# Kernel optimization log

Measured on AMD Instinct MI355X. Metric: run time of the kernel, lower is better.

## Reference

```python
import jax, jax.numpy as jnp
import numpy as np

NUM_HEADS = 8
WIN = 4
DIM = 256
EPS = 1e-5


def setup_inputs() -> dict:
    key = jax.random.key(0)
    ks = jax.random.split(key, 5)
    B, C, H, W = 2, DIM, 64, 64
    features = jax.random.normal(ks[0], (B, C, H, W), dtype=jnp.float32)
    # Linear(dim, 3*dim): stored as [C, 3C] so y = x @ qkv_w + qkv_b (matches torch x @ W.T + b)
    qkv_w = jax.random.normal(ks[1], (C, 3 * C), dtype=jnp.float32) * 0.02
    qkv_b = jax.random.normal(ks[2], (3 * C,), dtype=jnp.float32) * 0.02
    out_w = jax.random.normal(ks[3], (C, C), dtype=jnp.float32) * 0.02
    out_b = jax.random.normal(ks[4], (C,), dtype=jnp.float32) * 0.02
    ln_w = jnp.ones((C,), dtype=jnp.float32)
    ln_b = jnp.zeros((C,), dtype=jnp.float32)
    return {"features": features, "qkv_w": qkv_w, "qkv_b": qkv_b,
            "out_w": out_w, "out_b": out_b, "ln_w": ln_w, "ln_b": ln_b}


def reference(features, qkv_w, qkv_b, out_w, out_b, ln_w, ln_b):
    ws = WIN
    B, C, H, W = features.shape
    hc, wc = H // ws, W // ws          # windows per col / row (H,W divisible by ws)
    nW = hc * wc
    Tq = ws * ws
    h, d = NUM_HEADS, C // NUM_HEADS

    # --- query windows: replicate torch unfold(k=ws, s=ws).transpose(1,2).reshape(.., Tq, C)
    # torch unfold layout per window is (c, ki, kj); the reshape reinterprets that flat
    # C*ws*ws vector as [ws*ws, C]. A contiguous reshape reproduces this exactly.
    qwin = features.reshape(B, C, hc, ws, wc, ws).transpose(0, 2, 4, 1, 3, 5)  # [B,hc,wc,C,ws,ws]
    q_tok = qwin.reshape(B, nW, Tq, C)
    # LayerNorm(dim) on query tokens only
    mu = q_tok.mean(-1, keepdims=True)
    var = ((q_tok - mu) ** 2).mean(-1, keepdims=True)
    q_tok = (q_tok - mu) / jnp.sqrt(var + EPS) * ln_w + ln_b

    # --- local KV: unfold(k=2*ws, s=ws) on features padded by ws//2 each side
    lk = 2 * ws
    p = ws // 2
    fp = jnp.pad(features, ((0, 0), (0, 0), (p, p), (p, p)))
    rows = jnp.arange(hc)[:, None] * ws + jnp.arange(lk)[None, :]  # [hc, lk]
    cols = jnp.arange(wc)[:, None] * ws + jnp.arange(lk)[None, :]  # [wc, lk]
    loc = fp[:, :, rows[:, None, :, None], cols[None, :, None, :]]  # [B,C,hc,wc,lk,lk]
    loc = loc.transpose(0, 2, 3, 1, 4, 5).reshape(B, nW, lk * lk, C)  # same layout replica
    Ll = lk * lk

    # --- pooled KV (computed once per batch; the torch expand is a pure broadcast)
    mid = features.reshape(B, C, H // 2, 2, W // 2, 2).mean(axis=(3, 5))
    glb = features.reshape(B, C, H // 4, 4, W // 4, 4).mean(axis=(3, 5))
    mid_tok = mid.reshape(B, C, -1).transpose(0, 2, 1)   # [B, Lm, C]
    glb_tok = glb.reshape(B, C, -1).transpose(0, 2, 1)   # [B, Lg, C]
    Lm = mid_tok.shape[1]

    # --- shared qkv projection; queries use only the Q slice, KV use only K/V slices
    q = (q_tok @ qkv_w + qkv_b)[..., :C]

    def kv(t):
        o = t @ qkv_w + qkv_b
        return o[..., C:2 * C], o[..., 2 * C:]

    kl, vl = kv(loc)
    km, vm = kv(mid_tok)
    kg, vg = kv(glb_tok)

    # heads
    q = q.reshape(B, nW, Tq, h, d).transpose(0, 1, 3, 2, 4)           # [B,nW,h,Tq,d]
    kl = kl.reshape(B, nW, Ll, h, d).transpose(0, 1, 3, 2, 4)
    vl = vl.reshape(B, nW, Ll, h, d).transpose(0, 1, 3, 2, 4)
    km = km.reshape(B, Lm, h, d).transpose(0, 2, 1, 3)                # [B,h,Lm,d]
    vm = vm.reshape(B, Lm, h, d).transpose(0, 2, 1, 3)
    kg = kg.reshape(B, -1, h, d).transpose(0, 2, 1, 3)
    vg = vg.reshape(B, -1, h, d).transpose(0, 2, 1, 3)

    scale = 1.0 / np.sqrt(d).astype(np.float32)
    s_l = jnp.einsum('bwhqd,bwhkd->bwhqk', q, kl)
    s_m = jnp.einsum('bwhqd,bhkd->bwhqk', q, km)
    s_g = jnp.einsum('bwhqd,bhkd->bwhqk', q, kg)
    attn = jax.nn.softmax(jnp.concatenate([s_l, s_m, s_g], axis=-1) * scale, axis=-1)
    a_l = attn[..., :Ll]
    a_m = attn[..., Ll:Ll + Lm]
    a_g = attn[..., Ll + Lm:]
    o = (jnp.einsum('bwhqk,bwhkd->bwhqd', a_l, vl)
         + jnp.einsum('bwhqk,bhkd->bwhqd', a_m, vm)
         + jnp.einsum('bwhqk,bhkd->bwhqd', a_g, vg))

    o = o.transpose(0, 1, 3, 2, 4).reshape(B, nW, Tq, C)
    o = o @ out_w + out_b
    # restore spatial layout: view(B,hc,wc,ws,ws,C).permute(0,5,1,3,2,4).view(B,C,H,W)
    o = o.reshape(B, hc, wc, ws, ws, C).transpose(0, 5, 1, 3, 2, 4).reshape(B, C, H, W)
    return o + features
```

## Files before the change

kernel.cpp:

```cpp
#include <hip/hip_runtime.h>
#include <math.h>

#define HWSZ 4096
#define QSCALE_L2E 0.25501988932587245f

typedef __bf16 bf16x2 __attribute__((ext_vector_type(2)));
typedef __bf16 bf16x4 __attribute__((ext_vector_type(4)));
typedef __bf16 bf16x8 __attribute__((ext_vector_type(8)));
typedef float  f32x4  __attribute__((ext_vector_type(4)));

__global__ __launch_bounds__(256) void fused_pre(
    const float* __restrict__ F, const float* __restrict__ lnw,
    const float* __restrict__ lnb, __bf16* __restrict__ qnb,
    float* __restrict__ mid, float* __restrict__ glb,
    const float* __restrict__ Wqkv, const float* __restrict__ Wout,
    __bf16* __restrict__ WT, __bf16* __restrict__ WoT)
{
  __shared__ float sbuf[64*68];
  int u = blockIdx.x;
  int tid = threadIdx.x;
  if (u < 512) {
    float* sm = sbuf;
    int blk = u;
    int b = blk >> 8, wy = (blk >> 4) & 15, t = blk & 15;
    const float* Fb = F + ((size_t)(b*256 + t*16))*HWSZ + (wy*4)*64;
    int py = tid >> 6, x = tid & 63;
    #pragma unroll
    for (int j = 0; j < 16; ++j)
      sm[j*269 + py*67 + x] = Fb[(size_t)j*HWSZ + py*64 + x];
    __syncthreads();
    int wx = tid >> 4, cl = tid & 15;
    float vals[16], s1 = 0.f, s2 = 0.f;
    #pragma unroll
    for (int p = 0; p < 16; ++p) {
      float v = sm[cl*269 + (p >> 2)*67 + wx*4 + (p & 3)];
      vals[p] = v; s1 += v; s2 += v*v;
    }
    #pragma unroll
    for (int m = 1; m < 16; m <<= 1) { s1 += __shfl_xor(s1, m); s2 += __shfl_xor(s2, m); }
    float mean = s1 * (1.f/256.f);
    float var  = s2 * (1.f/256.f) - mean*mean;
    float rstd = rsqrtf(var + 1e-5f);
    __bf16* outp = qnb + (((size_t)(b*256 + wy*16 + wx))*16 + t)*256 + cl*16;
    bf16x8 o0, o1;
    #pragma unroll
    for (int p = 0; p < 8; ++p) {
      o0[p] = (__bf16)((vals[p]  -mean)*rstd*lnw[cl*16+p]   + lnb[cl*16+p]);
      o1[p] = (__bf16)((vals[p+8]-mean)*rstd*lnw[cl*16+p+8] + lnb[cl*16+p+8]);
    }
    *(bf16x8*)outp = o0;
    *(bf16x8*)(outp+8) = o1;
  } else if (u < 1024) {
    int bc = u - 512;
    int gy = tid >> 4, gx = tid & 15;
    const float* p = F + (size_t)bc*HWSZ + (gy*4)*64 + gx*4;
    float4 r0 = *(const float4*)(p);
    float4 r1 = *(const float4*)(p + 64);
    float4 r2 = *(const float4*)(p + 128);
    float4 r3 = *(const float4*)(p + 192);
    float m00 = 0.25f*(r0.x + r0.y + r1.x + r1.y);
    float m01 = 0.25f*(r0.z + r0.w + r1.z + r1.w);
    float m10 = 0.25f*(r2.x + r2.y + r3.x + r3.y);
    float m11 = 0.25f*(r2.z + r2.w + r3.z + r3.w);
    float* mp = mid + (size_t)bc*1024 + (gy*2)*32 + gx*2;
    *(float2*)mp        = make_float2(m00, m01);
    *(float2*)(mp + 32) = make_float2(m10, m11);
    glb[(size_t)bc*256 + gy*16 + gx] = 0.25f*(m00 + m01 + m10 + m11);
  } else {
    float (*T)[68] = (float(*)[68])sbuf;
    int v = u - 1024;
    int bx = v & 15, k0 = (v >> 4)*64;
    int c4 = (tid & 15)*4, rr = tid >> 4;
    const float* W; __bf16* D; int ncols, n0;
    if (bx < 12) { W = Wqkv; D = WT;  ncols = 768; n0 = bx*64; }
    else         { W = Wout; D = WoT; ncols = 256; n0 = (bx-12)*64; }
    #pragma unroll
    for (int p = 0; p < 4; ++p) {
      int row = p*16 + rr;
      float4 vv = *(const float4*)(W + (size_t)(k0+row)*ncols + n0 + c4);
      T[c4+0][row] = vv.x; T[c4+1][row] = vv.y; T[c4+2][row] = vv.z; T[c4+3][row] = vv.w;
    }
    __syncthreads();
    #pragma unroll
    for (int p = 0; p < 4; ++p) {
      int cc = p*16 + rr;
      bf16x4 o;
      o[0] = (__bf16)T[cc][c4+0]; o[1] = (__bf16)T[cc][c4+1];
      o[2] = (__bf16)T[cc][c4+2]; o[3] = (__bf16)T[cc][c4+3];
      *(bf16x4*)(D + (size_t)(n0+cc)*256 + k0 + c4) = o;
    }
  }
}

__global__ __launch_bounds__(256) void mgt_transpose(
    const float* __restrict__ mid, const float* __restrict__ glb,
    __bf16* __restrict__ mgt)
{
  __shared__ float T[64][68];
  int tt = blockIdx.x;
  int tid = threadIdx.x;
  int c4 = (tid & 15)*4, rr = tid >> 4;
  int b = tt / 20, tq = tt % 20;
  int t0 = tq*64, c0 = blockIdx.y*64;
  const float* src; int stride, toff;
  if (t0 < 1024) { src = mid + ((size_t)(b*256 + c0))*1024; stride = 1024; toff = t0; }
  else           { src = glb + ((size_t)(b*256 + c0))*256;  stride = 256;  toff = t0 - 1024; }
  #pragma unroll
  for (int p = 0; p < 4; ++p) {
    int row = p*16 + rr;
    float4 v = *(const float4*)(src + (size_t)row*stride + toff + c4);
    T[c4+0][row] = v.x; T[c4+1][row] = v.y; T[c4+2][row] = v.z; T[c4+3][row] = v.w;
  }
  __syncthreads();
  #pragma unroll
  for (int p = 0; p < 4; ++p) {
    int t2 = p*16 + rr;
    bf16x4 o;
    o[0] = (__bf16)T[t2][c4+0]; o[1] = (__bf16)T[t2][c4+1];
    o[2] = (__bf16)T[t2][c4+2]; o[3] = (__bf16)T[t2][c4+3];
    *(bf16x4*)(mgt + ((size_t)b*1280 + t0 + t2)*256 + c0 + c4) = o;
  }
}

__global__ __launch_bounds__(256) void fused_gemms(
    const float* __restrict__ F, const __bf16* __restrict__ qnb,
    const __bf16* __restrict__ mgt, const __bf16* __restrict__ WT,
    const float* __restrict__ qkvb,
    __bf16* __restrict__ qbf, __bf16* __restrict__ kloc,
    __bf16* __restrict__ vloct, __bf16* __restrict__ kmg,
    __bf16* __restrict__ vmgt)
{
  __shared__ __bf16 Bs[2][16*264];
  int u = blockIdx.x;
  int tid = threadIdx.x;
  int wv = tid >> 6, lane = tid & 63;
  int col = lane & 15, quad = lane >> 4;
  const f32x4 zero = {0.f,0.f,0.f,0.f};

  if (u < 512) {
    int bw = u;
    int b = bw >> 8, w = bw & 255;
    int wy = w >> 4, wx = w & 15;
    int m0 = wv*16;

    bf16x8 af[8];
    int x0 = wx*4 - 2;
    bool p0ok = (wx > 0), p3ok = (wx < 15);
    const float* Fb = F + ((size_t)(b*256 + 4*(m0+col)))*HWSZ;
    #pragma unroll
    for (int kk = 0; kk < 8; ++kk) {
      int r = kk >> 1;
      int y = wy*4 + (kk & 1)*4 + quad - 2;
      bool yok = ((unsigned)y < 64u);
      const float* row = Fb + (size_t)r*HWSZ + y*64 + x0;
      float2 v0 = make_float2(0.f,0.f), v1 = make_float2(0.f,0.f);
      float2 v2 = make_float2(0.f,0.f), v3 = make_float2(0.f,0.f);
      if (yok) {
        if (p0ok) v0 = *(const float2*)(row);
        v1 = *(const float2*)(row + 2);
        v2 = *(const float2*)(row + 4);
        if (p3ok) v3 = *(const float2*)(row + 6);
      }
      af[kk][0] = (__bf16)v0.x; af[kk][1] = (__bf16)v0.y;
      af[kk][2] = (__bf16)v1.x; af[kk][3] = (__bf16)v1.y;
      af[kk][4] = (__bf16)v2.x; af[kk][5] = (__bf16)v2.y;
      af[kk][6] = (__bf16)v3.x; af[kk][7] = (__bf16)v3.y;
    }

    int brow = tid >> 4, bseg = tid & 15;
    const __bf16* wsrc = WT + ((size_t)(256 + brow))*256 + bseg*16;
    __bf16* bd0 = &Bs[0][0] + brow*264 + bseg*16;
    {
      bf16x8 a0 = *(const bf16x8*)wsrc;
      bf16x8 a1 = *(const bf16x8*)(wsrc + 8);
      *(bf16x8*)bd0 = a0;
      *(bf16x8*)(bd0 + 8) = a1;
    }
    bf16x8 g0 = *(const bf16x8*)(wsrc + (size_t)4096);
    bf16x8 g1 = *(const bf16x8*)(wsrc + (size_t)4096 + 8);
    __syncthreads();

    #pragma unroll 1
    for (int nt = 0; nt < 32; ++nt) {
      if (nt < 31) {
        __bf16* d = &Bs[(nt+1) & 1][0] + brow*264 + bseg*16;
        *(bf16x8*)d = g0;
        *(bf16x8*)(d + 8) = g1;
      }
      if (nt < 30) {
        const __bf16* p = wsrc + (size_t)(nt+2)*4096;
        g0 = *(const bf16x8*)p;
        g1 = *(const bf16x8*)(p + 8);
      }
      int n = nt*16 + col;
      float bias_n = qkvb[256 + n];
      const __bf16* Bb = &Bs[nt & 1][0] + col*264 + quad*8;
      f32x4 acc = zero;
      #pragma unroll
      for (int kk = 0; kk < 8; ++kk) {
        bf16x8 bv = *(const bf16x8*)(Bb + kk*32);
        acc = __builtin_amdgcn_mfma_f32_16x16x32_bf16(af[kk], bv, acc, 0, 0, 0);
      }
      if (nt < 16) {
        #pragma unroll
        for (int r = 0; r < 4; ++r)
          kloc[((size_t)bw*64 + m0 + quad*4 + r)*256 + n] = (__bf16)(acc[r] + bias_n);
      } else {
        bf16x4 o;
        #pragma unroll
        for (int r = 0; r < 4; ++r) o[r] = (__bf16)(acc[r] + bias_n);
        *(bf16x4*)(vloct + ((size_t)bw*256 + (n - 256))*64 + m0 + quad*4) = o;
      }
      __syncthreads();
    }
  } else if (u < 768) {
    int blk = u - 512;
    int tb = blk >> 1, nh = blk & 1;
    int n0 = nh*128;
    int m0 = tb*64 + wv*16;

    bf16x8 bq[8];
    const __bf16* qp = qnb + ((size_t)(m0 + col))*256 + quad*8;
    #pragma unroll
    for (int kk = 0; kk < 8; ++kk) bq[kk] = *(const bf16x8*)(qp + kk*32);

    int brow = tid >> 4, bseg = tid & 15;
    const __bf16* wsrc = WT + ((size_t)(n0 + brow))*256 + bseg*16;
    {
      bf16x8 a0 = *(const bf16x8*)wsrc;
      bf16x8 a1 = *(const bf16x8*)(wsrc + 8);
      __bf16* d = &Bs[0][0] + brow*264 + bseg*16;
      *(bf16x8*)d = a0; *(bf16x8*)(d + 8) = a1;
    }
    bf16x8 g0 = *(const bf16x8*)(wsrc + (size_t)4096);
    bf16x8 g1 = *(const bf16x8*)(wsrc + (size_t)4096 + 8);
    __syncthreads();

    #pragma unroll 1
    for (int s = 0; s < 8; ++s) {
      if (s < 7) {
        __bf16* d = &Bs[(s+1) & 1][0] + brow*264 + bseg*16;
        *(bf16x8*)d = g0; *(bf16x8*)(d + 8) = g1;
      }
      if (s < 6) {
        const __bf16* p = wsrc + (size_t)(s+2)*4096;
        g0 = *(const bf16x8*)p; g1 = *(const bf16x8*)(p + 8);
      }
      const __bf16* Ab = &Bs[s & 1][0] + col*264 + quad*8;
      f32x4 acc = zero;
      #pragma unroll
      for (int kk = 0; kk < 8; ++kk) {
        bf16x8 wf = *(const bf16x8*)(Ab + kk*32);
        acc = __builtin_amdgcn_mfma_f32_16x16x32_bf16(wf, bq[kk], acc, 0, 0, 0);
      }
      int nq4 = n0 + s*16 + quad*4;
      float4 b4 = *(const float4*)(qkvb + nq4);
      float bb[4] = {b4.x, b4.y, b4.z, b4.w};
      bf16x4 o;
      #pragma unroll
      for (int r = 0; r < 4; ++r) o[r] = (__bf16)((acc[r]+bb[r])*QSCALE_L2E);
      *(bf16x4*)(qbf + ((size_t)(m0 + col))*256 + nq4) = o;
      __syncthreads();
    }
  } else {
    int v = u - 768;
    int tb = v % 20, nq = (v / 20) & 3, b = v / 80;
    int m0 = tb*64 + wv*16;
    int n0 = nq*128;

    const __bf16* Ab = mgt + ((size_t)b*1280 + m0 + col)*256 + quad*8;
    bf16x8 af[8];
    #pragma unroll
    for (int kk = 0; kk < 8; ++kk) af[kk] = *(const bf16x8*)(Ab + kk*32);

    int brow = tid >> 4, bseg = tid & 15;
    const __bf16* wsrc = WT + ((size_t)(256 + n0 + brow))*256 + bseg*16;
    {
      bf16x8 a0 = *(const bf16x8*)wsrc;
      bf16x8 a1 = *(const bf16x8*)(wsrc + 8);
      __bf16* d = &Bs[0][0] + brow*264 + bseg*16;
      *(bf16x8*)d = a0; *(bf16x8*)(d + 8) = a1;
    }
    bf16x8 g0 = *(const bf16x8*)(wsrc + (size_t)4096);
    bf16x8 g1 = *(const bf16x8*)(wsrc + (size_t)4096 + 8);
    __syncthreads();

    #pragma unroll 1
    for (int s = 0; s < 8; ++s) {
      if (s < 7) {
        __bf16* d = &Bs[(s+1) & 1][0] + brow*264 + bseg*16;
        *(bf16x8*)d = g0; *(bf16x8*)(d + 8) = g1;
      }
      if (s < 6) {
        const __bf16* p = wsrc + (size_t)(s+2)*4096;
        g0 = *(const bf16x8*)p; g1 = *(const bf16x8*)(p + 8);
      }
      int n = n0 + s*16 + col;
      float bias_n = qkvb[256 + n];
      const __bf16* Bb = &Bs[s & 1][0] + col*264 + quad*8;
      f32x4 acc = zero;
      #pragma unroll
      for (int kk = 0; kk < 8; ++kk) {
        bf16x8 bv = *(const bf16x8*)(Bb + kk*32);
        acc = __builtin_amdgcn_mfma_f32_16x16x32_bf16(af[kk], bv, acc, 0, 0, 0);
      }
      if (n < 256) {
        #pragma unroll
        for (int r = 0; r < 4; ++r)
          kmg[((size_t)b*1280 + m0 + quad*4 + r)*256 + n] = (__bf16)(acc[r] + bias_n);
      } else {
        bf16x4 o;
        #pragma unroll
        for (int r = 0; r < 4; ++r) o[r] = (__bf16)(acc[r] + bias_n);
        *(bf16x4*)(vmgt + ((size_t)b*256 + (n - 256))*1280 + m0 + quad*4) = o;
      }
      __syncthreads();
    }
  }
}

__global__ __launch_bounds__(512) void attn_mfma(
    const __bf16* __restrict__ qbf, const __bf16* __restrict__ kloc,
    const __bf16* __restrict__ vloct, const __bf16* __restrict__ kmg,
    const __bf16* __restrict__ vmgt, __bf16* __restrict__ obf)
{
  __shared__ __bf16 Ks[2][64][40];
  __shared__ __bf16 Vs[2][32][72];
  int blk = blockIdx.x;
  int b = blk >> 8, rr = blk & 255;
  int h = rr >> 5, wg = rr & 31;
  int tid = threadIdx.x, wv = tid >> 6, lane = tid & 63;
  int col = lane & 15, quad = lane >> 4;
  int bw = b*256 + wg*8 + wv;

  bool isK = tid < 256;
  int krow = tid >> 2,        kseg = tid & 3;
  int vrow = (tid - 256) >> 3, vseg = (tid - 256) & 7;
  const __bf16* gbase;
  __bf16 *l0, *l1;
  size_t gslab;
  if (isK) {
    gbase = kmg + ((size_t)(b*1280 + krow))*256 + h*32 + kseg*8;
    gslab = (size_t)64*256;
    l0 = &Ks[0][krow][kseg*8]; l1 = &Ks[1][krow][kseg*8];
  } else {
    gbase = vmgt + ((size_t)(b*256 + h*32 + vrow))*1280 + vseg*8;
    gslab = 64;
    l0 = &Vs[0][vrow][vseg*8]; l1 = &Vs[1][vrow][vseg*8];
  }

  bf16x8 aq = *(const bf16x8*)(qbf + ((size_t)(bw*16 + col))*256 + h*32 + quad*8);
  f32x4 O0 = {0.f,0.f,0.f,0.f}, O1 = {0.f,0.f,0.f,0.f};
  const f32x4 zero = {0.f,0.f,0.f,0.f};
  float ls = 0.f;

  bf16x8 sreg = *(const bf16x8*)gbase;

  const __bf16* klocb = kloc  + (size_t)bw*16384 + h*32 + quad*8;
  const __bf16* vlocb = vloct + (size_t)bw*16384 + (size_t)(h*32)*64;
  #pragma unroll
  for (int ch = 0; ch < 2; ++ch) {
    bf16x8 k0 = *(const bf16x8*)(klocb + (size_t)(ch*32 + col)*256);
    bf16x8 k1 = *(const bf16x8*)(klocb + (size_t)(ch*32 + 16 + col)*256);
    bf16x4 va0 = *(const bf16x4*)(vlocb + (size_t)col*64      + ch*32 + quad*4);
    bf16x4 va1 = *(const bf16x4*)(vlocb + (size_t)col*64      + ch*32 + 16 + quad*4);
    bf16x4 vb0 = *(const bf16x4*)(vlocb + (size_t)(16+col)*64 + ch*32 + quad*4);
    bf16x4 vb1 = *(const bf16x4*)(vlocb + (size_t)(16+col)*64 + ch*32 + 16 + quad*4);
    f32x4 S0 = __builtin_amdgcn_mfma_f32_16x16x32_bf16(k0, aq, zero, 0, 0, 0);
    f32x4 S1 = __builtin_amdgcn_mfma_f32_16x16x32_bf16(k1, aq, zero, 0, 0, 0);
    bf16x8 pf;
    #pragma unroll
    for (int r = 0; r < 4; ++r) {
      float p0 = __builtin_amdgcn_exp2f(S0[r]);
      float p1 = __builtin_amdgcn_exp2f(S1[r]);
      ls += p0 + p1;
      pf[r] = (__bf16)p0; pf[4+r] = (__bf16)p1;
    }
    bf16x8 v0 = __builtin_shufflevector(va0, va1, 0,1,2,3,4,5,6,7);
    bf16x8 v1 = __builtin_shufflevector(vb0, vb1, 0,1,2,3,4,5,6,7);
    O0 = __builtin_amdgcn_mfma_f32_16x16x32_bf16(pf, v0, O0, 0, 0, 0);
    O1 = __builtin_amdgcn_mfma_f32_16x16x32_bf16(pf, v1, O1, 0, 0, 0);
  }

  *(bf16x8*)l0 = sreg;
  sreg = *(const bf16x8*)(gbase + gslab);
  __syncthreads();

  #pragma unroll 1
  for (int s = 0; s < 20; ++s) {
    if (s + 1 < 20) {
      __bf16* ld = (s & 1) ? l0 : l1;
      *(bf16x8*)ld = sreg;
      if (s + 2 < 20) sreg = *(const bf16x8*)(gbase + (size_t)(s+2)*gslab);
    }
    const __bf16* Kb = &Ks[s & 1][0][0];
    const __bf16* Vb = &Vs[s & 1][0][0];
    #pragma unroll
    for (int c = 0; c < 2; ++c) {
      bf16x8 k0 = *(const bf16x8*)(Kb + (c*32 + col)*40 + quad*8);
      bf16x8 k1 = *(const bf16x8*)(Kb + (c*32 + 16 + col)*40 + quad*8);
      bf16x4 va0 = *(const bf16x4*)(Vb + (size_t)col*72      + c*32 + quad*4);
      bf16x4 va1 = *(const bf16x4*)(Vb + (size_t)col*72      + c*32 + 16 + quad*4);
      bf16x4 vb0 = *(const bf16x4*)(Vb + (size_t)(16+col)*72 + c*32 + quad*4);
      bf16x4 vb1 = *(const bf16x4*)(Vb + (size_t)(16+col)*72 + c*32 + 16 + quad*4);
      f32x4 S0 = __builtin_amdgcn_mfma_f32_16x16x32_bf16(k0, aq, zero, 0, 0, 0);
      f32x4 S1 = __builtin_amdgcn_mfma_f32_16x16x32_bf16(k1, aq, zero, 0, 0, 0);
      bf16x8 pf;
      #pragma unroll
      for (int r = 0; r < 4; ++r) {
        float p0 = __builtin_amdgcn_exp2f(S0[r]);
        float p1 = __builtin_amdgcn_exp2f(S1[r]);
        ls += p0 + p1;
        pf[r] = (__bf16)p0; pf[4+r] = (__bf16)p1;
      }
      bf16x8 v0 = __builtin_shufflevector(va0, va1, 0,1,2,3,4,5,6,7);
      bf16x8 v1 = __builtin_shufflevector(vb0, vb1, 0,1,2,3,4,5,6,7);
      O0 = __builtin_amdgcn_mfma_f32_16x16x32_bf16(pf, v0, O0, 0, 0, 0);
      O1 = __builtin_amdgcn_mfma_f32_16x16x32_bf16(pf, v1, O1, 0, 0, 0);
    }
    __syncthreads();
  }

  ls += __shfl_xor(ls, 16);
  ls += __shfl_xor(ls, 32);
  __bf16* op = obf + ((size_t)(bw*16) + quad*4)*256 + h*32 + col;
  #pragma unroll
  for (int r = 0; r < 4; ++r) {
    float inv = 1.f / __shfl(ls, quad*4 + r);
    op[(size_t)r*256]      = (__bf16)(O0[r]*inv);
    op[(size_t)r*256 + 16] = (__bf16)(O1[r]*inv);
  }
}

__global__ __launch_bounds__(256) void gemm_out_strip(
    const __bf16* __restrict__ obf, const __bf16* __restrict__ WoT,
    const float* __restrict__ outb, const float* __restrict__ Fres,
    float* __restrict__ Out)
{
  __shared__ __bf16 Bs4[4*16*264];
  __shared__ __bf16 strip[64*264];
  int blk = blockIdx.x;
  int b = blk >> 7, rest = blk & 127;
  int wy = rest >> 3, cq = (rest >> 1) & 3, xh = rest & 1;
  int c0 = cq*64;
  int tid = threadIdx.x, wv = tid >> 6, lane = tid & 63;
  int col = lane & 15, quad = lane >> 4;
  const f32x4 zero = {0.f,0.f,0.f,0.f};

  {
    int brow = tid >> 4, bseg = tid & 15;
    const __bf16* wsrc = WoT + ((size_t)(c0 + brow))*256 + bseg*16;
    #pragma unroll
    for (int s = 0; s < 4; ++s) {
      bf16x8 a0 = *(const bf16x8*)(wsrc + (size_t)s*4096);
      bf16x8 a1 = *(const bf16x8*)(wsrc + (size_t)s*4096 + 8);
      __bf16* d = Bs4 + s*4224 + brow*264 + bseg*16;
      *(bf16x8*)d = a0; *(bf16x8*)(d + 8) = a1;
    }
  }
  __syncthreads();

  #pragma unroll
  for (int i = 0; i < 2; ++i) {
    int wx = xh*8 + wv*2 + i;
    int win = b*256 + wy*16 + wx;
    bf16x8 ao[8];
    const __bf16* op = obf + ((size_t)win*16 + col)*256 + quad*8;
    #pragma unroll
    for (int kk = 0; kk < 8; ++kk) ao[kk] = *(const bf16x8*)(op + kk*32);
    #pragma unroll
    for (int nt = 0; nt < 4; ++nt) {
      const __bf16* Bb = Bs4 + nt*4224 + col*264 + quad*8;
      f32x4 acc = zero;
      #pragma unroll
      for (int kk = 0; kk < 8; ++kk) {
        bf16x8 wf = *(const bf16x8*)(Bb + kk*32);
        acc = __builtin_amdgcn_mfma_f32_16x16x32_bf16(ao[kk], wf, acc, 0, 0, 0);
      }
      bf16x4 o;
      #pragma unroll
      for (int r = 0; r < 4; ++r) o[r] = (__bf16)acc[r];
      *(bf16x4*)&strip[(nt*16+col)*264 + quad*66 + wx*4] = o;
    }
  }
  __syncthreads();
  #pragma unroll
  for (int j = 0; j < 8; ++j) {
    int f4 = j*256 + tid;
    int xq = (f4 & 7) + xh*8, y = (f4 >> 3) & 3, c = f4 >> 5;
    bf16x4 d = *(const bf16x4*)&strip[c*264 + y*66 + xq*4];
    size_t off = ((size_t)(b*256 + c0 + c))*HWSZ + (wy*4 + y)*64 + xq*4;
    float4 r4 = *(const float4*)(Fres + off);
    float bn = outb[c0 + c];
    float4 o;
    o.x = (float)d[0] + bn + r4.x; o.y = (float)d[1] + bn + r4.y;
    o.z = (float)d[2] + bn + r4.z; o.w = (float)d[3] + bn + r4.w;
    *(float4*)(Out + off) = o;
  }
}

extern "C" void kernel_launch(void* const* d_in, const int* in_sizes, int n_in,
                              void* d_out, int out_size, void* d_ws, size_t ws_size,
                              hipStream_t stream) {
  const float* F     = (const float*)d_in[0];
  const float* qkv_w = (const float*)d_in[1];
  const float* qkv_b = (const float*)d_in[2];
  const float* out_w = (const float*)d_in[3];
  const float* out_b = (const float*)d_in[4];
  const float* ln_w  = (const float*)d_in[5];
  const float* ln_b  = (const float*)d_in[6];
  float* out = (float*)d_out;

  __bf16* qnb   = (__bf16*)d_ws;
  __bf16* qbf   = qnb   + 2097152;
  __bf16* obf   = qbf   + 2097152;
  __bf16* kloc  = obf   + 2097152;
  __bf16* vloct = kloc  + 8388608;
  __bf16* kmg   = vloct + 8388608;
  __bf16* vmgt  = kmg   + 655360;
  __bf16* mgt   = vmgt  + 655360;
  __bf16* WT    = mgt   + 655360;
  __bf16* WoT   = WT    + 196608;
  float*  mid   = (float*)(WoT + 65536);
  float*  glb   = mid   + 524288;

  fused_pre<<<1088, 256, 0, stream>>>(F, ln_w, ln_b, qnb, mid, glb,
                                      qkv_w, out_w, WT, WoT);
  mgt_transpose<<<dim3(40, 4), 256, 0, stream>>>(mid, glb, mgt);
  fused_gemms<<<928, 256, 0, stream>>>(F, qnb, mgt, WT, qkv_b,
                                       qbf, kloc, vloct, kmg, vmgt);
  attn_mfma<<<512, 512, 0, stream>>>(qbf, kloc, vloct, kmg, vmgt, obf);
  gemm_out_strip<<<256, 256, 0, stream>>>(obf, WoT, out_b, F, out);
}
```

Baseline: 147.0 us.

## Fuse mgt transpose into GEMM A-loads and process two windows per block

Removes the separate mgt_transpose kernel. The pooled/global KV GEMM blocks now read fp32 mid/glb directly with strided scalar loads and convert to bf16 in registers. The local KV GEMM blocks each handle two adjacent windows, so every B tile staged in shared memory is reused for twice the MFMA work and the grid shrinks. This saves one launch and an intermediate buffer round trip. In exchange the strided scalar global loads are uncoalesced and the doubled A fragments raise register pressure.

```diff
diff --git a/kernel.cpp b/kernel.cpp
--- a/kernel.cpp
+++ b/kernel.cpp
@@ -92,40 +92,10 @@
   }
 }
 
-__global__ __launch_bounds__(256) void mgt_transpose(
-    const float* __restrict__ mid, const float* __restrict__ glb,
-    __bf16* __restrict__ mgt)
-{
-  __shared__ float T[64][68];
-  int tt = blockIdx.x;
-  int tid = threadIdx.x;
-  int c4 = (tid & 15)*4, rr = tid >> 4;
-  int b = tt / 20, tq = tt % 20;
-  int t0 = tq*64, c0 = blockIdx.y*64;
-  const float* src; int stride, toff;
-  if (t0 < 1024) { src = mid + ((size_t)(b*256 + c0))*1024; stride = 1024; toff = t0; }
-  else           { src = glb + ((size_t)(b*256 + c0))*256;  stride = 256;  toff = t0 - 1024; }
-  #pragma unroll
-  for (int p = 0; p < 4; ++p) {
-    int row = p*16 + rr;
-    float4 v = *(const float4*)(src + (size_t)row*stride + toff + c4);
-    T[c4+0][row] = v.x; T[c4+1][row] = v.y; T[c4+2][row] = v.z; T[c4+3][row] = v.w;
-  }
-  __syncthreads();
-  #pragma unroll
-  for (int p = 0; p < 4; ++p) {
-    int t2 = p*16 + rr;
-    bf16x4 o;
-    o[0] = (__bf16)T[t2][c4+0]; o[1] = (__bf16)T[t2][c4+1];
-    o[2] = (__bf16)T[t2][c4+2]; o[3] = (__bf16)T[t2][c4+3];
-    *(bf16x4*)(mgt + ((size_t)b*1280 + t0 + t2)*256 + c0 + c4) = o;
-  }
-}
-
 __global__ __launch_bounds__(256) void fused_gemms(
     const float* __restrict__ F, const __bf16* __restrict__ qnb,
-    const __bf16* __restrict__ mgt, const __bf16* __restrict__ WT,
-    const float* __restrict__ qkvb,
+    const float* __restrict__ mid, const float* __restrict__ glb,
+    const __bf16* __restrict__ WT, const float* __restrict__ qkvb,
     __bf16* __restrict__ qbf, __bf16* __restrict__ kloc,
     __bf16* __restrict__ vloct, __bf16* __restrict__ kmg,
     __bf16* __restrict__ vmgt)
@@ -137,34 +107,37 @@
   int col = lane & 15, quad = lane >> 4;
   const f32x4 zero = {0.f,0.f,0.f,0.f};
 
-  if (u < 512) {
-    int bw = u;
-    int b = bw >> 8, w = bw & 255;
-    int wy = w >> 4, wx = w & 15;
+  if (u < 256) {
+    int b = u >> 7, wpair = u & 127;
+    int wy = wpair >> 3, wx0 = (wpair & 7)*2;
     int m0 = wv*16;
 
-    bf16x8 af[8];
-    int x0 = wx*4 - 2;
-    bool p0ok = (wx > 0), p3ok = (wx < 15);
+    bf16x8 af[2][8];
     const float* Fb = F + ((size_t)(b*256 + 4*(m0+col)))*HWSZ;
     #pragma unroll
-    for (int kk = 0; kk < 8; ++kk) {
-      int r = kk >> 1;
-      int y = wy*4 + (kk & 1)*4 + quad - 2;
-      bool yok = ((unsigned)y < 64u);
-      const float* row = Fb + (size_t)r*HWSZ + y*64 + x0;
-      float2 v0 = make_float2(0.f,0.f), v1 = make_float2(0.f,0.f);
-      float2 v2 = make_float2(0.f,0.f), v3 = make_float2(0.f,0.f);
-      if (yok) {
-        if (p0ok) v0 = *(const float2*)(row);
-        v1 = *(const float2*)(row + 2);
-        v2 = *(const float2*)(row + 4);
-        if (p3ok) v3 = *(const float2*)(row + 6);
-      }
-      af[kk][0] = (__bf16)v0.x; af[kk][1] = (__bf16)v0.y;
-      af[kk][2] = (__bf16)v1.x; af[kk][3] = (__bf16)v1.y;
-      af[kk][4] = (__bf16)v2.x; af[kk][5] = (__bf16)v2.y;
-      af[kk][6] = (__bf16)v3.x; af[kk][7] = (__bf16)v3.y;
+    for (int wi = 0; wi < 2; ++wi) {
+      int wx = wx0 + wi;
+      int x0 = wx*4 - 2;
+      bool p0ok = (wx > 0), p3ok = (wx < 15);
+      #pragma unroll
+      for (int kk = 0; kk < 8; ++kk) {
+        int r = kk >> 1;
+        int y = wy*4 + (kk & 1)*4 + quad - 2;
+        bool yok = ((unsigned)y < 64u);
+        const float* row = Fb + (size_t)r*HWSZ + y*64 + x0;
+        float2 v0 = make_float2(0.f,0.f), v1 = make_float2(0.f,0.f);
+        float2 v2 = make_float2(0.f,0.f), v3 = make_float2(0.f,0.f);
+        if (yok) {
+          if (p0ok) v0 = *(const float2*)(row);
+          v1 = *(const float2*)(row + 2);
+          v2 = *(const float2*)(row + 4);
+          if (p3ok) v3 = *(const float2*)(row + 6);
+        }
+        af[wi][kk][0] = (__bf16)v0.x; af[wi][kk][1] = (__bf16)v0.y;
+        af[wi][kk][2] = (__bf16)v1.x; af[wi][kk][3] = (__bf16)v1.y;
+        af[wi][kk][4] = (__bf16)v2.x; af[wi][kk][5] = (__bf16)v2.y;
+        af[wi][kk][6] = (__bf16)v3.x; af[wi][kk][7] = (__bf16)v3.y;
+      }
     }
 
     int brow = tid >> 4, bseg = tid & 15;
@@ -195,26 +168,34 @@
       int n = nt*16 + col;
       float bias_n = qkvb[256 + n];
       const __bf16* Bb = &Bs[nt & 1][0] + col*264 + quad*8;
-      f32x4 acc = zero;
+      f32x4 acc0 = zero, acc1 = zero;
       #pragma unroll
       for (int kk = 0; kk < 8; ++kk) {
         bf16x8 bv = *(const bf16x8*)(Bb + kk*32);
-        acc = __builtin_amdgcn_mfma_f32_16x16x32_bf16(af[kk], bv, acc, 0, 0, 0);
-      }
+        acc0 = __builtin_amdgcn_mfma_f32_16x16x32_bf16(af[0][kk], bv, acc0, 0, 0, 0);
+        acc1 = __builtin_amdgcn_mfma_f32_16x16x32_bf16(af[1][kk], bv, acc1, 0, 0, 0);
+      }
+      size_t bw0 = (size_t)(b*256 + wy*16 + wx0);
       if (nt < 16) {
         #pragma unroll
-        for (int r = 0; r < 4; ++r)
-          kloc[((size_t)bw*64 + m0 + quad*4 + r)*256 + n] = (__bf16)(acc[r] + bias_n);
+        for (int r = 0; r < 4; ++r) {
+          kloc[(bw0*64       + m0 + quad*4 + r)*256 + n] = (__bf16)(acc0[r] + bias_n);
+          kloc[((bw0+1)*64   + m0 + quad*4 + r)*256 + n] = (__bf16)(acc1[r] + bias_n);
+        }
       } else {
-        bf16x4 o;
+        bf16x4 o0, o1;
         #pragma unroll
-        for (int r = 0; r < 4; ++r) o[r] = (__bf16)(acc[r] + bias_n);
-        *(bf16x4*)(vloct + ((size_t)bw*256 + (n - 256))*64 + m0 + quad*4) = o;
+        for (int r = 0; r < 4; ++r) {
+          o0[r] = (__bf16)(acc0[r] + bias_n);
+          o1[r] = (__bf16)(acc1[r] + bias_n);
+        }
+        *(bf16x4*)(vloct + (bw0*256     + (n - 256))*64 + m0 + quad*4) = o0;
+        *(bf16x4*)(vloct + ((bw0+1)*256 + (n - 256))*64 + m0 + quad*4) = o1;
       }
       __syncthreads();
     }
-  } else if (u < 768) {
-    int blk = u - 512;
+  } else if (u < 512) {
+    int blk = u - 256;
     int tb = blk >> 1, nh = blk & 1;
     int n0 = nh*128;
     int m0 = tb*64 + wv*16;
@@ -263,15 +244,29 @@
       __syncthreads();
     }
   } else {
-    int v = u - 768;
+    int v = u - 512;
     int tb = v % 20, nq = (v / 20) & 3, b = v / 80;
     int m0 = tb*64 + wv*16;
     int n0 = nq*128;
 
-    const __bf16* Ab = mgt + ((size_t)b*1280 + m0 + col)*256 + quad*8;
     bf16x8 af[8];
-    #pragma unroll
-    for (int kk = 0; kk < 8; ++kk) af[kk] = *(const bf16x8*)(Ab + kk*32);
+    if (tb < 16) {
+      const float* Abase = mid + ((size_t)(b*256))*1024 + (m0 + col);
+      #pragma unroll
+      for (int kk = 0; kk < 8; ++kk) {
+        #pragma unroll
+        for (int j = 0; j < 8; ++j)
+          af[kk][j] = (__bf16)Abase[(size_t)(kk*32 + quad*8 + j)*1024];
+      }
+    } else {
+      const float* Abase = glb + ((size_t)(b*256))*256 + (m0 - 1024 + col);
+      #pragma unroll
+      for (int kk = 0; kk < 8; ++kk) {
+        #pragma unroll
+        for (int j = 0; j < 8; ++j)
+          af[kk][j] = (__bf16)Abase[(size_t)(kk*32 + quad*8 + j)*256];
+      }
+    }
 
     int brow = tid >> 4, bseg = tid & 15;
     const __bf16* wsrc = WT + ((size_t)(256 + n0 + brow))*256 + bseg*16;
@@ -518,16 +513,14 @@
   __bf16* vloct = kloc  + 8388608;
   __bf16* kmg   = vloct + 8388608;
   __bf16* vmgt  = kmg   + 655360;
-  __bf16* mgt   = vmgt  + 655360;
-  __bf16* WT    = mgt   + 655360;
+  __bf16* WT    = vmgt  + 655360;
   __bf16* WoT   = WT    + 196608;
   float*  mid   = (float*)(WoT + 65536);
   float*  glb   = mid   + 524288;
 
   fused_pre<<<1088, 256, 0, stream>>>(F, ln_w, ln_b, qnb, mid, glb,
                                       qkv_w, out_w, WT, WoT);
-  mgt_transpose<<<dim3(40, 4), 256, 0, stream>>>(mid, glb, mgt);
-  fused_gemms<<<928, 256, 0, stream>>>(F, qnb, mgt, WT, qkv_b,
+  fused_gemms<<<672, 256, 0, stream>>>(F, qnb, mid, glb, WT, qkv_b,
                                        qbf, kloc, vloct, kmg, vmgt);
   attn_mfma<<<512, 512, 0, stream>>>(qbf, kloc, vloct, kmg, vmgt, obf);
   gemm_out_strip<<<256, 256, 0, stream>>>(obf, WoT, out_b, F, out);
```

Measured after the change: 144.7 us. Within noise of the previous version (-1.6%).
